# Performance work log

Hardware: AMD Instinct MI355X
Metric: run time of the kernel (lower is better)

## Reference

```python
import jax, jax.numpy as jnp
import numpy as np

FWD_TRUNCATION = 0.05
EPS_LOG = 1e-20


def setup_inputs() -> dict:
    key = jax.random.key(0)
    k1, k2, k3, k4, k5 = jax.random.split(key, 5)
    B, N, M = 32768, 1024, 64
    samples = jax.random.normal(k1, (B, M), dtype=jnp.float32)
    mask = jax.random.uniform(k2, (B, M), dtype=jnp.float32)
    centroids = jax.random.normal(k3, (N, M), dtype=jnp.float32)
    # sd kept away from 0 to avoid huge 1/sd scaling
    sd = jax.random.uniform(k4, (1, M), dtype=jnp.float32) + 0.5
    log_marginal = jax.random.normal(k5, (1, N), dtype=jnp.float32)
    return {"samples": samples, "mask": mask, "centroids": centroids,
            "sd": sd, "log_marginal": log_marginal}


def _masked_pairwise_sq_distances(A, B, mask):
    # A: [B, M] samples, B: [N, M] centroids, mask: [B, M]
    sq_mask = mask * mask
    mA = mask * A
    A_d = jnp.sum(mA * mA, axis=1, keepdims=True)            # [B, 1]
    B_d = sq_mask @ (B * B).T                                 # [B, N]
    cross = (sq_mask * A) @ B.T                                # [B, N]
    return jax.nn.relu(A_d - 2.0 * cross + B_d)               # [B, N]


def _pdf_truncate(pdf, truncation):
    # discretePdfTruncate: zero out entries below truncation * rowmax, renormalize
    threshold = truncation * jnp.max(pdf, axis=-1, keepdims=True)
    pdf = jax.nn.relu(jnp.sign(pdf - threshold)) * pdf
    return pdf / jnp.sum(pdf, axis=-1, keepdims=True)


def reference(samples, mask, centroids, sd, log_marginal):
    # Mahalanobis: fold 1/sd into the mask (sqMahalanobisDistances)
    m = mask / sd
    dist = _masked_pairwise_sq_distances(samples, centroids, m)  # [B, N]
    log_prior = jax.nn.log_softmax(log_marginal, axis=-1)        # [1, N]
    logits = log_prior - 0.5 * dist                              # [B, N]
    # softmaxWithTemperature (temperature=1) -> truncate -> renormalize
    pdf = jax.nn.softmax(logits, axis=-1)
    pdf = _pdf_truncate(pdf, FWD_TRUNCATION)
    log_pdf = jnp.log(pdf + EPS_LOG)                             # logPdfTruncate
    return pdf, log_pdf
```

## Files before the change

kernel.cpp:

```cpp
#include <hip/hip_runtime.h>
#include <math.h>

#define N_C 1024
#define M_F 64
#define B_R 32768
#define R_B 32
#define LDX 132

typedef short bf16x8 __attribute__((ext_vector_type(8)));
typedef float f32x4 __attribute__((ext_vector_type(4)));

__device__ __forceinline__ short f2bf(float x) {
  unsigned b = __float_as_uint(x);
  b += 0x7fffu + ((b >> 16) & 1u);
  return (short)(b >> 16);
}
__device__ __forceinline__ float bf2f(short h) {
  return __uint_as_float(((unsigned)(unsigned short)h) << 16);
}

__global__ void logprior_kernel(const float* __restrict__ lm, float* __restrict__ lp) {
  __shared__ float red[256];
  const int t = threadIdx.x;
  float v[4];
  float mx = -INFINITY;
#pragma unroll
  for (int i = 0; i < 4; ++i) { v[i] = lm[i * 256 + t]; mx = fmaxf(mx, v[i]); }
  red[t] = mx;
  __syncthreads();
  for (int s = 128; s > 0; s >>= 1) {
    if (t < s) red[t] = fmaxf(red[t], red[t + s]);
    __syncthreads();
  }
  mx = red[0];
  __syncthreads();
  float sum = 0.f;
#pragma unroll
  for (int i = 0; i < 4; ++i) { v[i] -= mx; sum += expf(v[i]); }
  red[t] = sum;
  __syncthreads();
  for (int s = 128; s > 0; s >>= 1) {
    if (t < s) red[t] += red[t + s];
    __syncthreads();
  }
  const float l = logf(red[0]);
#pragma unroll
  for (int i = 0; i < 4; ++i) lp[i * 256 + t] = v[i] - l;
}

__global__ void prep_y(const float* __restrict__ centroids,
                       bf16x8* __restrict__ yh, bf16x8* __restrict__ ym,
                       bf16x8* __restrict__ yl) {
  const int tid = blockIdx.x * 256 + threadIdx.x;
  const int l = tid & 63;
  const int c = (tid >> 6) & 63;
  const int s = tid >> 12;
  const int n = c * 16 + (l & 15);
  const int k0 = s * 32 + (l >> 4) * 8;
  bf16x8 h, mid, lo;
#pragma unroll
  for (int j = 0; j < 8; ++j) {
    const int k = k0 + j;
    float y;
    if (k < 64) {
      y = centroids[n * M_F + k];
    } else {
      const float cc = centroids[n * M_F + (k - 64)];
      y = cc * cc;
    }
    const short hh = f2bf(y);
    const float r1 = y - bf2f(hh);
    const short mm = f2bf(r1);
    const float r2 = r1 - bf2f(mm);
    h[j] = hh;
    mid[j] = mm;
    lo[j] = f2bf(r2);
  }
  const int blob = (s * 64 + c) * 64 + l;
  yh[blob] = h;
  ym[blob] = mid;
  yl[blob] = lo;
}

__global__ __launch_bounds__(512, 2) void rmm_main(
    const float* __restrict__ samples, const float* __restrict__ mask,
    const float* __restrict__ sd, const float* __restrict__ lp_g,
    const bf16x8* __restrict__ yh_g, const bf16x8* __restrict__ ym_g,
    const bf16x8* __restrict__ yl_g, float* __restrict__ out) {
  __shared__ float xs[R_B * LDX];
  __shared__ float lp_s[N_C];
  __shared__ float ad_s[R_B];
  __shared__ float red_s[R_B * 8];

  const int t = threadIdx.x;
  const int b0 = blockIdx.x * R_B;
  const int w = t >> 6;
  const int l = t & 63;
  const int m = l & 15;
  const int q = l >> 4;

  if (t < 256) *(float4*)(lp_s + (t << 2)) = *(const float4*)(lp_g + (t << 2));

  {
    const int r = t >> 4;
    const int j4 = (t & 15) << 2;
    const float4 s4 = *(const float4*)(samples + (size_t)(b0 + r) * M_F + j4);
    const float4 m4 = *(const float4*)(mask + (size_t)(b0 + r) * M_F + j4);
    const float4 d4 = *(const float4*)(sd + j4);
    const float sa[4] = {s4.x, s4.y, s4.z, s4.w};
    const float ma[4] = {m4.x, m4.y, m4.z, m4.w};
    const float da[4] = {d4.x, d4.y, d4.z, d4.w};
    float ad = 0.f;
#pragma unroll
    for (int k = 0; k < 4; ++k) {
      const float mm = ma[k] / da[k];
      const float uu = mm * mm;
      const float mA = mm * sa[k];
      ad = fmaf(mA, mA, ad);
      xs[r * LDX + j4 + k] = -2.0f * (uu * sa[k]);
      xs[r * LDX + 64 + j4 + k] = uu;
    }
#pragma unroll
    for (int off = 1; off < 16; off <<= 1) ad += __shfl_xor(ad, off, 64);
    if ((t & 15) == 0) ad_s[r] = ad;
  }

  f32x4 acc[2][8];
#pragma unroll
  for (int mt = 0; mt < 2; ++mt)
#pragma unroll
    for (int c = 0; c < 8; ++c) acc[mt][c] = (f32x4){0.f, 0.f, 0.f, 0.f};

  __syncthreads();

  const int sx[8] = {1, 2, 0, 1, 2, 0, 1, 0};
  const int sy[8] = {2, 1, 2, 1, 0, 1, 0, 0};

#pragma unroll 1
  for (int s = 0; s < 4; ++s) {
    const size_t sbase = (size_t)(s * 64 + w * 8) * 64 + l;
    const bf16x8* yh = yh_g + sbase;
    const bf16x8* ym = ym_g + sbase;
    const bf16x8* yl = yl_g + sbase;

    bf16x8 B[3][2][2];
#pragma unroll
    for (int tl = 0; tl < 2; ++tl) {
      B[0][0][tl] = yh[tl * 64];
      B[1][0][tl] = ym[tl * 64];
      B[2][0][tl] = yl[tl * 64];
    }

    bf16x8 A[3][2];
#pragma unroll
    for (int mt = 0; mt < 2; ++mt) {
      const float* xp = &xs[(mt * 16 + m) * LDX + s * 32 + q * 8];
      float av[8];
      *(float4*)&av[0] = *(const float4*)xp;
      *(float4*)&av[4] = *(const float4*)(xp + 4);
      bf16x8 ah, amd, alo;
#pragma unroll
      for (int j = 0; j < 8; ++j) {
        const short hh = f2bf(av[j]);
        const float r1 = av[j] - bf2f(hh);
        const short mm = f2bf(r1);
        const float r2 = r1 - bf2f(mm);
        ah[j] = hh;
        amd[j] = mm;
        alo[j] = f2bf(r2);
      }
      A[0][mt] = ah;
      A[1][mt] = amd;
      A[2][mt] = alo;
    }

#pragma unroll
    for (int p = 0; p < 4; ++p) {
      const int cur = p & 1;
      const int nxt = cur ^ 1;
      if (p < 3) {
#pragma unroll
        for (int tl = 0; tl < 2; ++tl) {
          B[0][nxt][tl] = yh[(2 * (p + 1) + tl) * 64];
          B[1][nxt][tl] = ym[(2 * (p + 1) + tl) * 64];
          B[2][nxt][tl] = yl[(2 * (p + 1) + tl) * 64];
        }
      }
#pragma unroll
      for (int sp = 0; sp < 8; ++sp)
#pragma unroll
        for (int tl = 0; tl < 2; ++tl)
#pragma unroll
          for (int mt = 0; mt < 2; ++mt)
            acc[mt][2 * p + tl] = __builtin_amdgcn_mfma_f32_16x16x32_bf16(
                A[sx[sp]][mt], B[sy[sp]][cur][tl], acc[mt][2 * p + tl], 0, 0, 0);
    }
  }

  float adv[2][4];
#pragma unroll
  for (int mt = 0; mt < 2; ++mt)
#pragma unroll
    for (int g = 0; g < 4; ++g) adv[mt][g] = ad_s[mt * 16 + q * 4 + g];
  float lpv[8];
#pragma unroll
  for (int c = 0; c < 8; ++c) lpv[c] = lp_s[w * 128 + c * 16 + m];

#pragma unroll
  for (int mt = 0; mt < 2; ++mt)
#pragma unroll
    for (int c = 0; c < 8; ++c)
#pragma unroll
      for (int g = 0; g < 4; ++g) {
        const float dist = fmaxf(adv[mt][g] + acc[mt][c][g], 0.0f);
        acc[mt][c][g] = lpv[c] - 0.5f * dist;
      }

  float mx[2][4];
#pragma unroll
  for (int mt = 0; mt < 2; ++mt)
#pragma unroll
    for (int g = 0; g < 4; ++g) {
      float v = acc[mt][0][g];
#pragma unroll
      for (int c = 1; c < 8; ++c) v = fmaxf(v, acc[mt][c][g]);
#pragma unroll
      for (int off = 1; off < 16; off <<= 1) v = fmaxf(v, __shfl_xor(v, off, 64));
      mx[mt][g] = v;
    }
  if (m == 0) {
#pragma unroll
    for (int mt = 0; mt < 2; ++mt)
#pragma unroll
      for (int g = 0; g < 4; ++g) red_s[(mt * 16 + q * 4 + g) * 8 + w] = mx[mt][g];
  }
  __syncthreads();
#pragma unroll
  for (int mt = 0; mt < 2; ++mt)
#pragma unroll
    for (int g = 0; g < 4; ++g) {
      const int row = mt * 16 + q * 4 + g;
      const float4 r0 = *(const float4*)(&red_s[row * 8]);
      const float4 r1 = *(const float4*)(&red_s[row * 8 + 4]);
      mx[mt][g] = fmaxf(fmaxf(fmaxf(r0.x, r0.y), fmaxf(r0.z, r0.w)),
                        fmaxf(fmaxf(r1.x, r1.y), fmaxf(r1.z, r1.w)));
    }
  __syncthreads();

  float sm[2][4];
#pragma unroll
  for (int mt = 0; mt < 2; ++mt)
#pragma unroll
    for (int g = 0; g < 4; ++g) {
      float ssum = 0.f;
#pragma unroll
      for (int c = 0; c < 8; ++c) {
        const float e = expf(acc[mt][c][g] - mx[mt][g]);
        acc[mt][c][g] = e;
        ssum += e;
      }
#pragma unroll
      for (int off = 1; off < 16; off <<= 1) ssum += __shfl_xor(ssum, off, 64);
      sm[mt][g] = ssum;
    }
  if (m == 0) {
#pragma unroll
    for (int mt = 0; mt < 2; ++mt)
#pragma unroll
      for (int g = 0; g < 4; ++g) red_s[(mt * 16 + q * 4 + g) * 8 + w] = sm[mt][g];
  }
  __syncthreads();
#pragma unroll
  for (int mt = 0; mt < 2; ++mt)
#pragma unroll
    for (int g = 0; g < 4; ++g) {
      const int row = mt * 16 + q * 4 + g;
      const float4 r0 = *(const float4*)(&red_s[row * 8]);
      const float4 r1 = *(const float4*)(&red_s[row * 8 + 4]);
      sm[mt][g] = ((r0.x + r0.y) + (r0.z + r0.w)) + ((r1.x + r1.y) + (r1.z + r1.w));
    }
  __syncthreads();

  float thr[2][4], qs[2][4];
#pragma unroll
  for (int mt = 0; mt < 2; ++mt)
#pragma unroll
    for (int g = 0; g < 4; ++g) {
      const float S1 = sm[mt][g];
      thr[mt][g] = 0.05f * (1.0f / S1);
      float s2 = 0.f;
#pragma unroll
      for (int c = 0; c < 8; ++c) {
        const float p = acc[mt][c][g] / S1;
        acc[mt][c][g] = p;
        s2 += (p > thr[mt][g]) ? p : 0.0f;
      }
#pragma unroll
      for (int off = 1; off < 16; off <<= 1) s2 += __shfl_xor(s2, off, 64);
      qs[mt][g] = s2;
    }
  if (m == 0) {
#pragma unroll
    for (int mt = 0; mt < 2; ++mt)
#pragma unroll
      for (int g = 0; g < 4; ++g) red_s[(mt * 16 + q * 4 + g) * 8 + w] = qs[mt][g];
  }
  __syncthreads();
#pragma unroll
  for (int mt = 0; mt < 2; ++mt)
#pragma unroll
    for (int g = 0; g < 4; ++g) {
      const int row = mt * 16 + q * 4 + g;
      const float4 r0 = *(const float4*)(&red_s[row * 8]);
      const float4 r1 = *(const float4*)(&red_s[row * 8 + 4]);
      qs[mt][g] = ((r0.x + r0.y) + (r0.z + r0.w)) + ((r1.x + r1.y) + (r1.z + r1.w));
    }

  const size_t colbase = (size_t)(w * 128 + m);
#pragma unroll
  for (int mt = 0; mt < 2; ++mt)
#pragma unroll
    for (int g = 0; g < 4; ++g) {
      float* orow = out + (size_t)(b0 + mt * 16 + q * 4 + g) * N_C + colbase;
      float* lrow = orow + (size_t)B_R * N_C;
#pragma unroll
      for (int c = 0; c < 8; ++c) {
        const float p = acc[mt][c][g];
        const float pf = (p > thr[mt][g]) ? (p / qs[mt][g]) : 0.0f;
        orow[c * 16] = pf;
        lrow[c * 16] = logf(pf + 1e-20f);
      }
    }
}

extern "C" void kernel_launch(void* const* d_in, const int* in_sizes, int n_in,
                              void* d_out, int out_size, void* d_ws, size_t ws_size,
                              hipStream_t stream) {
  const float* samples   = (const float*)d_in[0];
  const float* mask      = (const float*)d_in[1];
  const float* centroids = (const float*)d_in[2];
  const float* sd        = (const float*)d_in[3];
  const float* lm        = (const float*)d_in[4];
  float* out = (float*)d_out;

  char* ws = (char*)d_ws;
  float* lp  = (float*)ws;
  bf16x8* yh = (bf16x8*)(ws + 4096);
  bf16x8* ym = (bf16x8*)(ws + 4096 + 262144);
  bf16x8* yl = (bf16x8*)(ws + 4096 + 2 * 262144);

  logprior_kernel<<<1, 256, 0, stream>>>(lm, lp);
  prep_y<<<64, 256, 0, stream>>>(centroids, yh, ym, yl);
  rmm_main<<<B_R / R_B, 512, 0, stream>>>(samples, mask, sd, lp, yh, ym, yl, out);
}
```

Before: 377.8 us.

## Halve waves per block, widen per-wave columns, cheaper bf16 split and fast math

Block size drops from 512 to 256 threads, so each wave now computes 256 centroid columns with 16 accumulator tiles, and the cross-wave reductions shrink to 4 entries. The three-way bf16 split of the sample operand now uses bit truncation and packing instead of round-to-nearest conversions. expf/logf become __expf/__logf, and the per-element division becomes a reciprocal multiply. These cut VALU work and reduction overhead, at the cost of higher register pressure and fewer resident waves.

```diff
diff --git a/kernel.cpp b/kernel.cpp
--- a/kernel.cpp
+++ b/kernel.cpp
@@ -9,6 +9,7 @@
 
 typedef short bf16x8 __attribute__((ext_vector_type(8)));
 typedef float f32x4 __attribute__((ext_vector_type(4)));
+typedef unsigned int uint4v __attribute__((ext_vector_type(4)));
 
 __device__ __forceinline__ short f2bf(float x) {
   unsigned b = __float_as_uint(x);
@@ -17,6 +18,28 @@
 }
 __device__ __forceinline__ float bf2f(short h) {
   return __uint_as_float(((unsigned)(unsigned short)h) << 16);
+}
+
+__device__ __forceinline__ void split3(const float* f, bf16x8& h, bf16x8& m, bf16x8& l) {
+  uint4v hp, mp, lp;
+#pragma unroll
+  for (int i = 0; i < 4; ++i) {
+    const unsigned b0 = __float_as_uint(f[2 * i]);
+    const unsigned b1 = __float_as_uint(f[2 * i + 1]);
+    const unsigned h0 = b0 & 0xFFFF0000u, h1 = b1 & 0xFFFF0000u;
+    const float r0 = f[2 * i] - __uint_as_float(h0);
+    const float r1 = f[2 * i + 1] - __uint_as_float(h1);
+    hp[i] = (b0 >> 16) | h1;
+    const unsigned rb0 = __float_as_uint(r0), rb1 = __float_as_uint(r1);
+    const unsigned m0 = rb0 & 0xFFFF0000u, m1 = rb1 & 0xFFFF0000u;
+    const float s0 = r0 - __uint_as_float(m0);
+    const float s1 = r1 - __uint_as_float(m1);
+    mp[i] = (rb0 >> 16) | m1;
+    lp[i] = (__float_as_uint(s0) >> 16) | (__float_as_uint(s1) & 0xFFFF0000u);
+  }
+  h = __builtin_bit_cast(bf16x8, hp);
+  m = __builtin_bit_cast(bf16x8, mp);
+  l = __builtin_bit_cast(bf16x8, lp);
 }
 
 __global__ void logprior_kernel(const float* __restrict__ lm, float* __restrict__ lp) {
@@ -82,7 +105,7 @@
   yl[blob] = lo;
 }
 
-__global__ __launch_bounds__(512, 2) void rmm_main(
+__global__ __launch_bounds__(256, 2) void rmm_main(
     const float* __restrict__ samples, const float* __restrict__ mask,
     const float* __restrict__ sd, const float* __restrict__ lp_g,
     const bf16x8* __restrict__ yh_g, const bf16x8* __restrict__ ym_g,
@@ -90,7 +113,7 @@
   __shared__ float xs[R_B * LDX];
   __shared__ float lp_s[N_C];
   __shared__ float ad_s[R_B];
-  __shared__ float red_s[R_B * 8];
+  __shared__ float red_s[R_B * 4];
 
   const int t = threadIdx.x;
   const int b0 = blockIdx.x * R_B;
@@ -99,37 +122,40 @@
   const int m = l & 15;
   const int q = l >> 4;
 
-  if (t < 256) *(float4*)(lp_s + (t << 2)) = *(const float4*)(lp_g + (t << 2));
+  *(float4*)(lp_s + (t << 2)) = *(const float4*)(lp_g + (t << 2));
 
   {
-    const int r = t >> 4;
-    const int j4 = (t & 15) << 2;
-    const float4 s4 = *(const float4*)(samples + (size_t)(b0 + r) * M_F + j4);
-    const float4 m4 = *(const float4*)(mask + (size_t)(b0 + r) * M_F + j4);
-    const float4 d4 = *(const float4*)(sd + j4);
-    const float sa[4] = {s4.x, s4.y, s4.z, s4.w};
-    const float ma[4] = {m4.x, m4.y, m4.z, m4.w};
-    const float da[4] = {d4.x, d4.y, d4.z, d4.w};
+    const int r = t >> 3;
+    const int j8 = (t & 7) << 3;
+    const float* sp = samples + (size_t)(b0 + r) * M_F + j8;
+    const float* mp = mask + (size_t)(b0 + r) * M_F + j8;
+    float sa[8], ma[8], da[8];
+    *(float4*)&sa[0] = *(const float4*)sp;
+    *(float4*)&sa[4] = *(const float4*)(sp + 4);
+    *(float4*)&ma[0] = *(const float4*)mp;
+    *(float4*)&ma[4] = *(const float4*)(mp + 4);
+    *(float4*)&da[0] = *(const float4*)(sd + j8);
+    *(float4*)&da[4] = *(const float4*)(sd + j8 + 4);
     float ad = 0.f;
 #pragma unroll
-    for (int k = 0; k < 4; ++k) {
+    for (int k = 0; k < 8; ++k) {
       const float mm = ma[k] / da[k];
       const float uu = mm * mm;
       const float mA = mm * sa[k];
       ad = fmaf(mA, mA, ad);
-      xs[r * LDX + j4 + k] = -2.0f * (uu * sa[k]);
-      xs[r * LDX + 64 + j4 + k] = uu;
-    }
-#pragma unroll
-    for (int off = 1; off < 16; off <<= 1) ad += __shfl_xor(ad, off, 64);
-    if ((t & 15) == 0) ad_s[r] = ad;
-  }
-
-  f32x4 acc[2][8];
-#pragma unroll
-  for (int mt = 0; mt < 2; ++mt)
-#pragma unroll
-    for (int c = 0; c < 8; ++c) acc[mt][c] = (f32x4){0.f, 0.f, 0.f, 0.f};
+      xs[r * LDX + j8 + k] = -2.0f * (uu * sa[k]);
+      xs[r * LDX + 64 + j8 + k] = uu;
+    }
+#pragma unroll
+    for (int off = 1; off < 8; off <<= 1) ad += __shfl_xor(ad, off, 64);
+    if ((t & 7) == 0) ad_s[r] = ad;
+  }
+
+  f32x4 acc[2][16];
+#pragma unroll
+  for (int mt = 0; mt < 2; ++mt)
+#pragma unroll
+    for (int c = 0; c < 16; ++c) acc[mt][c] = (f32x4){0.f, 0.f, 0.f, 0.f};
 
   __syncthreads();
 
@@ -138,17 +164,17 @@
 
 #pragma unroll 1
   for (int s = 0; s < 4; ++s) {
-    const size_t sbase = (size_t)(s * 64 + w * 8) * 64 + l;
+    const size_t sbase = (size_t)(s * 64 + w * 16) * 64 + l;
     const bf16x8* yh = yh_g + sbase;
     const bf16x8* ym = ym_g + sbase;
     const bf16x8* yl = yl_g + sbase;
 
-    bf16x8 B[3][2][2];
-#pragma unroll
-    for (int tl = 0; tl < 2; ++tl) {
-      B[0][0][tl] = yh[tl * 64];
-      B[1][0][tl] = ym[tl * 64];
-      B[2][0][tl] = yl[tl * 64];
+    bf16x8 Bh[2], Bm[2], Bl[2];
+#pragma unroll
+    for (int p = 0; p < 2; ++p) {
+      Bh[p] = yh[p * 64];
+      Bm[p] = ym[p * 64];
+      Bl[p] = yl[p * 64];
     }
 
     bf16x8 A[3][2];
@@ -158,42 +184,26 @@
       float av[8];
       *(float4*)&av[0] = *(const float4*)xp;
       *(float4*)&av[4] = *(const float4*)(xp + 4);
-      bf16x8 ah, amd, alo;
-#pragma unroll
-      for (int j = 0; j < 8; ++j) {
-        const short hh = f2bf(av[j]);
-        const float r1 = av[j] - bf2f(hh);
-        const short mm = f2bf(r1);
-        const float r2 = r1 - bf2f(mm);
-        ah[j] = hh;
-        amd[j] = mm;
-        alo[j] = f2bf(r2);
-      }
-      A[0][mt] = ah;
-      A[1][mt] = amd;
-      A[2][mt] = alo;
-    }
-
-#pragma unroll
-    for (int p = 0; p < 4; ++p) {
-      const int cur = p & 1;
-      const int nxt = cur ^ 1;
-      if (p < 3) {
-#pragma unroll
-        for (int tl = 0; tl < 2; ++tl) {
-          B[0][nxt][tl] = yh[(2 * (p + 1) + tl) * 64];
-          B[1][nxt][tl] = ym[(2 * (p + 1) + tl) * 64];
-          B[2][nxt][tl] = yl[(2 * (p + 1) + tl) * 64];
-        }
-      }
-#pragma unroll
-      for (int sp = 0; sp < 8; ++sp)
-#pragma unroll
-        for (int tl = 0; tl < 2; ++tl)
-#pragma unroll
-          for (int mt = 0; mt < 2; ++mt)
-            acc[mt][2 * p + tl] = __builtin_amdgcn_mfma_f32_16x16x32_bf16(
-                A[sx[sp]][mt], B[sy[sp]][cur][tl], acc[mt][2 * p + tl], 0, 0, 0);
+      split3(av, A[0][mt], A[1][mt], A[2][mt]);
+    }
+
+#pragma unroll
+    for (int c = 0; c < 16; ++c) {
+      const int cur = c & 1;
+      const bf16x8 bh = Bh[cur], bm = Bm[cur], bl = Bl[cur];
+      if (c < 14) {
+        Bh[cur] = yh[(c + 2) * 64];
+        Bm[cur] = ym[(c + 2) * 64];
+        Bl[cur] = yl[(c + 2) * 64];
+      }
+#pragma unroll
+      for (int sp = 0; sp < 8; ++sp) {
+        const bf16x8 bb = (sy[sp] == 0) ? bh : ((sy[sp] == 1) ? bm : bl);
+#pragma unroll
+        for (int mt = 0; mt < 2; ++mt)
+          acc[mt][c] = __builtin_amdgcn_mfma_f32_16x16x32_bf16(
+              A[sx[sp]][mt], bb, acc[mt][c], 0, 0, 0);
+      }
     }
   }
 
@@ -202,14 +212,14 @@
   for (int mt = 0; mt < 2; ++mt)
 #pragma unroll
     for (int g = 0; g < 4; ++g) adv[mt][g] = ad_s[mt * 16 + q * 4 + g];
-  float lpv[8];
-#pragma unroll
-  for (int c = 0; c < 8; ++c) lpv[c] = lp_s[w * 128 + c * 16 + m];
-
-#pragma unroll
-  for (int mt = 0; mt < 2; ++mt)
-#pragma unroll
-    for (int c = 0; c < 8; ++c)
+  float lpv[16];
+#pragma unroll
+  for (int c = 0; c < 16; ++c) lpv[c] = lp_s[w * 256 + c * 16 + m];
+
+#pragma unroll
+  for (int mt = 0; mt < 2; ++mt)
+#pragma unroll
+    for (int c = 0; c < 16; ++c)
 #pragma unroll
       for (int g = 0; g < 4; ++g) {
         const float dist = fmaxf(adv[mt][g] + acc[mt][c][g], 0.0f);
@@ -223,7 +233,7 @@
     for (int g = 0; g < 4; ++g) {
       float v = acc[mt][0][g];
 #pragma unroll
-      for (int c = 1; c < 8; ++c) v = fmaxf(v, acc[mt][c][g]);
+      for (int c = 1; c < 16; ++c) v = fmaxf(v, acc[mt][c][g]);
 #pragma unroll
       for (int off = 1; off < 16; off <<= 1) v = fmaxf(v, __shfl_xor(v, off, 64));
       mx[mt][g] = v;
@@ -232,18 +242,15 @@
 #pragma unroll
     for (int mt = 0; mt < 2; ++mt)
 #pragma unroll
-      for (int g = 0; g < 4; ++g) red_s[(mt * 16 + q * 4 + g) * 8 + w] = mx[mt][g];
-  }
-  __syncthreads();
-#pragma unroll
-  for (int mt = 0; mt < 2; ++mt)
-#pragma unroll
-    for (int g = 0; g < 4; ++g) {
-      const int row = mt * 16 + q * 4 + g;
-      const float4 r0 = *(const float4*)(&red_s[row * 8]);
-      const float4 r1 = *(const float4*)(&red_s[row * 8 + 4]);
-      mx[mt][g] = fmaxf(fmaxf(fmaxf(r0.x, r0.y), fmaxf(r0.z, r0.w)),
-                        fmaxf(fmaxf(r1.x, r1.y), fmaxf(r1.z, r1.w)));
+      for (int g = 0; g < 4; ++g) red_s[(mt * 16 + q * 4 + g) * 4 + w] = mx[mt][g];
+  }
+  __syncthreads();
+#pragma unroll
+  for (int mt = 0; mt < 2; ++mt)
+#pragma unroll
+    for (int g = 0; g < 4; ++g) {
+      const float4 rv = *(const float4*)(&red_s[(mt * 16 + q * 4 + g) * 4]);
+      mx[mt][g] = fmaxf(fmaxf(rv.x, rv.y), fmaxf(rv.z, rv.w));
     }
   __syncthreads();
 
@@ -254,8 +261,8 @@
     for (int g = 0; g < 4; ++g) {
       float ssum = 0.f;
 #pragma unroll
-      for (int c = 0; c < 8; ++c) {
-        const float e = expf(acc[mt][c][g] - mx[mt][g]);
+      for (int c = 0; c < 16; ++c) {
+        const float e = __expf(acc[mt][c][g] - mx[mt][g]);
         acc[mt][c][g] = e;
         ssum += e;
       }
@@ -267,17 +274,15 @@
 #pragma unroll
     for (int mt = 0; mt < 2; ++mt)
 #pragma unroll
-      for (int g = 0; g < 4; ++g) red_s[(mt * 16 + q * 4 + g) * 8 + w] = sm[mt][g];
-  }
-  __syncthreads();
-#pragma unroll
-  for (int mt = 0; mt < 2; ++mt)
-#pragma unroll
-    for (int g = 0; g < 4; ++g) {
-      const int row = mt * 16 + q * 4 + g;
-      const float4 r0 = *(const float4*)(&red_s[row * 8]);
-      const float4 r1 = *(const float4*)(&red_s[row * 8 + 4]);
-      sm[mt][g] = ((r0.x + r0.y) + (r0.z + r0.w)) + ((r1.x + r1.y) + (r1.z + r1.w));
+      for (int g = 0; g < 4; ++g) red_s[(mt * 16 + q * 4 + g) * 4 + w] = sm[mt][g];
+  }
+  __syncthreads();
+#pragma unroll
+  for (int mt = 0; mt < 2; ++mt)
+#pragma unroll
+    for (int g = 0; g < 4; ++g) {
+      const float4 rv = *(const float4*)(&red_s[(mt * 16 + q * 4 + g) * 4]);
+      sm[mt][g] = (rv.x + rv.y) + (rv.z + rv.w);
     }
   __syncthreads();
 
@@ -290,7 +295,7 @@
       thr[mt][g] = 0.05f * (1.0f / S1);
       float s2 = 0.f;
 #pragma unroll
-      for (int c = 0; c < 8; ++c) {
+      for (int c = 0; c < 16; ++c) {
         const float p = acc[mt][c][g] / S1;
         acc[mt][c][g] = p;
         s2 += (p > thr[mt][g]) ? p : 0.0f;
@@ -303,32 +308,31 @@
 #pragma unroll
     for (int mt = 0; mt < 2; ++mt)
 #pragma unroll
-      for (int g = 0; g < 4; ++g) red_s[(mt * 16 + q * 4 + g) * 8 + w] = qs[mt][g];
-  }
-  __syncthreads();
-#pragma unroll
-  for (int mt = 0; mt < 2; ++mt)
-#pragma unroll
-    for (int g = 0; g < 4; ++g) {
-      const int row = mt * 16 + q * 4 + g;
-      const float4 r0 = *(const float4*)(&red_s[row * 8]);
-      const float4 r1 = *(const float4*)(&red_s[row * 8 + 4]);
-      qs[mt][g] = ((r0.x + r0.y) + (r0.z + r0.w)) + ((r1.x + r1.y) + (r1.z + r1.w));
-    }
-
-  const size_t colbase = (size_t)(w * 128 + m);
-#pragma unroll
-  for (int mt = 0; mt < 2; ++mt)
-#pragma unroll
-    for (int g = 0; g < 4; ++g) {
+      for (int g = 0; g < 4; ++g) red_s[(mt * 16 + q * 4 + g) * 4 + w] = qs[mt][g];
+  }
+  __syncthreads();
+#pragma unroll
+  for (int mt = 0; mt < 2; ++mt)
+#pragma unroll
+    for (int g = 0; g < 4; ++g) {
+      const float4 rv = *(const float4*)(&red_s[(mt * 16 + q * 4 + g) * 4]);
+      qs[mt][g] = (rv.x + rv.y) + (rv.z + rv.w);
+    }
+
+  const size_t colbase = (size_t)(w * 256 + m);
+#pragma unroll
+  for (int mt = 0; mt < 2; ++mt)
+#pragma unroll
+    for (int g = 0; g < 4; ++g) {
+      const float rq = 1.0f / qs[mt][g];
       float* orow = out + (size_t)(b0 + mt * 16 + q * 4 + g) * N_C + colbase;
       float* lrow = orow + (size_t)B_R * N_C;
 #pragma unroll
-      for (int c = 0; c < 8; ++c) {
+      for (int c = 0; c < 16; ++c) {
         const float p = acc[mt][c][g];
-        const float pf = (p > thr[mt][g]) ? (p / qs[mt][g]) : 0.0f;
+        const float pf = (p > thr[mt][g]) ? (p * rq) : 0.0f;
         orow[c * 16] = pf;
-        lrow[c * 16] = logf(pf + 1e-20f);
+        lrow[c * 16] = __logf(pf + 1e-20f);
       }
     }
 }
@@ -351,5 +355,5 @@
 
   logprior_kernel<<<1, 256, 0, stream>>>(lm, lp);
   prep_y<<<64, 256, 0, stream>>>(centroids, yh, ym, yl);
-  rmm_main<<<B_R / R_B, 512, 0, stream>>>(samples, mask, sd, lp, yh, ym, yl, out);
-}
+  rmm_main<<<B_R / R_B, 256, 0, stream>>>(samples, mask, sd, lp, yh, ym, yl, out);
+}
```

Result: faster. 335.1 us (-11.3%).
